# Kernel tuning notes

Hardware: AMD Instinct MI355X
Metric: run time of the kernel (lower is better)

The kernel has to match this reference:

```python
import jax, jax.numpy as jnp
import numpy as np

N_HEADS = 16


def setup_inputs() -> dict:
    key = jax.random.key(0)
    k1, k2, k3 = jax.random.split(key, 3)
    dim = 1024
    # ragged batch: 16 sequences with lengths 64..1024 (step 64), total_nnz = 8704
    lengths = np.arange(64, 1025, 64, dtype=np.int32)  # (16,)
    cu_seqlens = jnp.asarray(np.concatenate([[0], np.cumsum(lengths)]), dtype=jnp.int32)  # (17,)
    total_nnz = int(lengths.sum())  # 8704
    max_seqlen = int(lengths.max())  # 1024
    hidden_states = jax.random.normal(k1, (total_nnz, dim), dtype=jnp.float32)
    # nn.Linear(dim, 3*dim): weight (3*dim, dim), bias (3*dim)
    Wqkv_weight = jax.random.normal(k2, (3 * dim, dim), dtype=jnp.float32) * (dim ** -0.5)
    Wqkv_bias = jax.random.normal(k3, (3 * dim,), dtype=jnp.float32) * 0.02
    return {
        "hidden_states": hidden_states,
        "Wqkv_weight": Wqkv_weight,
        "Wqkv_bias": Wqkv_bias,
        "cu_seqlens": cu_seqlens,
        "max_seqlen": max_seqlen,
    }


def reference(hidden_states, Wqkv_weight, Wqkv_bias, cu_seqlens, max_seqlen):
    # Unpadded (varlen) self-attention, p_dropout = 0 (eval path).
    nnz, dim = hidden_states.shape
    H = N_HEADS
    D = dim // H
    S = int(max_seqlen)  # static pad length
    B = cu_seqlens.shape[0] - 1

    qkv = hidden_states @ Wqkv_weight.T + Wqkv_bias          # (nnz, 3*dim)
    qkv = qkv.reshape(nnz, 3, H, D)

    seqlens = cu_seqlens[1:] - cu_seqlens[:-1]                # (B,)
    pos = jnp.arange(S)
    valid = pos[None, :] < seqlens[:, None]                   # (B, S) token validity
    gather_idx = jnp.where(valid, cu_seqlens[:-1, None] + pos[None, :], 0)

    qkv_pad = qkv[gather_idx]                                 # (B, S, 3, H, D)
    q = qkv_pad[:, :, 0]                                      # (B, S, H, D)
    k = qkv_pad[:, :, 1]
    v = qkv_pad[:, :, 2]

    scale = 1.0 / jnp.sqrt(jnp.asarray(D, dtype=q.dtype))
    scores = jnp.einsum("bshd,bthd->bhst", q, k) * scale      # (B, H, S, S)
    neg_inf = jnp.asarray(-1e9, dtype=scores.dtype)
    scores = jnp.where(valid[:, None, None, :], scores, neg_inf)  # mask invalid keys
    attn = jax.nn.softmax(scores, axis=-1)
    out_pad = jnp.einsum("bhst,bthd->bshd", attn, v)          # (B, S, H, D)

    # scatter back to unpadded layout (nnz, H*D)
    tok = jnp.arange(nnz)
    tok_b = jnp.searchsorted(cu_seqlens, tok, side="right") - 1
    tok_s = tok - cu_seqlens[tok_b]
    out = out_pad[tok_b, tok_s].reshape(nnz, H * D)
    return out
```

## Files before the change

### kernel.cpp

```cpp
#include <hip/hip_runtime.h>
#include <math.h>


#define HD 64

typedef _Float16 half8 __attribute__((ext_vector_type(8)));
typedef _Float16 half4v __attribute__((ext_vector_type(4)));
typedef float f32x4 __attribute__((ext_vector_type(4)));

#define GLP(p) ((__attribute__((address_space(1))) void*)(p))
#define LDSP(p) ((__attribute__((address_space(3))) void*)(p))

__global__ __launch_bounds__(256)
void cvt_kernel(const float* __restrict__ A, const float* __restrict__ W,
                _Float16* __restrict__ Ah, _Float16* __restrict__ Wh,
                int nA4, int nW4)
{
    int total = nA4 + nW4;
    for (int i = blockIdx.x * blockDim.x + threadIdx.x; i < total;
         i += gridDim.x * blockDim.x) {
        const float* src; _Float16* dst; int j;
        if (i < nA4) { src = A; dst = Ah; j = i; }
        else         { src = W; dst = Wh; j = i - nA4; }
        float4 v = *(const float4*)(src + (size_t)j * 4);
        half4v h;
        h.x = (_Float16)v.x; h.y = (_Float16)v.y;
        h.z = (_Float16)v.z; h.w = (_Float16)v.w;
        *(half4v*)(dst + (size_t)j * 4) = h;
    }
}

__global__ __launch_bounds__(256)
void qkv_gemm_kernel(const _Float16* __restrict__ Ah, const _Float16* __restrict__ Wh,
                     const float* __restrict__ bias,
                     _Float16* __restrict__ Qo, _Float16* __restrict__ Ko,
                     _Float16* __restrict__ Vo,
                     int Kd, int dim)
{
    const int bm = blockIdx.x, bn = blockIdx.y;
    const int t = threadIdx.x;
    const int wid = t >> 6, lane = t & 63;
    const int wr = wid >> 1, wc = wid & 1;
    const int fr = lane & 15, fq = lane >> 4;

    __shared__ _Float16 As[128 * 64];
    __shared__ _Float16 Bs[128 * 64];

    const int m0 = bm * 128, n0 = bn * 128;

    f32x4 acc[4][4];
#pragma unroll
    for (int m = 0; m < 4; ++m)
#pragma unroll
        for (int n = 0; n < 4; ++n) acc[m][n] = (f32x4)0.f;

    float biasv[4];
#pragma unroll
    for (int n = 0; n < 4; ++n)
        biasv[n] = bias[n0 + wc * 64 + n * 16 + fr];

    int srow[4], slb[4];
#pragma unroll
    for (int i = 0; i < 4; ++i) {
        int c = t + 256 * i;
        srow[i] = c >> 3;
        slb[i]  = ((c & 7) << 4) ^ ((srow[i] & 7) << 4);
    }

    for (int k0 = 0; k0 < Kd; k0 += 64) {
        __syncthreads();
        {
            const char* Ab = (const char*)Ah + ((size_t)m0 * Kd + k0) * 2;
            const char* Bb = (const char*)Wh + ((size_t)n0 * Kd + k0) * 2;
#pragma unroll
            for (int i = 0; i < 4; ++i) {
                int phys = (t + 256 * i) * 16;
                __builtin_amdgcn_global_load_lds(GLP(Ab + (size_t)srow[i] * Kd * 2 + slb[i]),
                                                 LDSP((char*)As + phys), 16, 0, 0);
                __builtin_amdgcn_global_load_lds(GLP(Bb + (size_t)srow[i] * Kd * 2 + slb[i]),
                                                 LDSP((char*)Bs + phys), 16, 0, 0);
            }
        }
        __syncthreads();

#pragma unroll
        for (int kc = 0; kc < 2; ++kc) {
            half8 a[4], b[4];
#pragma unroll
            for (int m = 0; m < 4; ++m) {
                int row = wr * 64 + m * 16 + fr;
                a[m] = *(const half8*)((const char*)As + row * 128 +
                        ((kc * 64 + fq * 16) ^ ((fr & 7) << 4)));
            }
#pragma unroll
            for (int n = 0; n < 4; ++n) {
                int row = wc * 64 + n * 16 + fr;
                b[n] = *(const half8*)((const char*)Bs + row * 128 +
                        ((kc * 64 + fq * 16) ^ ((fr & 7) << 4)));
            }
#pragma unroll
            for (int m = 0; m < 4; ++m)
#pragma unroll
                for (int n = 0; n < 4; ++n)
                    acc[m][n] = __builtin_amdgcn_mfma_f32_16x16x32_f16(a[m], b[n], acc[m][n], 0, 0, 0);
        }
    }

    const int which = n0 / dim;
    const int offb  = n0 - which * dim;
    _Float16* dst = (which == 0) ? Qo : (which == 1) ? Ko : Vo;
#pragma unroll
    for (int m = 0; m < 4; ++m) {
#pragma unroll
        for (int n = 0; n < 4; ++n) {
            int gc = offb + wc * 64 + n * 16 + fr;
#pragma unroll
            for (int j = 0; j < 4; ++j) {
                int gm = m0 + wr * 64 + m * 16 + fq * 4 + j;
                dst[(size_t)gm * dim + gc] = (_Float16)(acc[m][n][j] + biasv[n]);
            }
        }
    }
}

__global__ __launch_bounds__(256)
void attn_kernel(const _Float16* __restrict__ Q, const _Float16* __restrict__ K,
                 const _Float16* __restrict__ V, const int* __restrict__ cu,
                 float* __restrict__ out, int dim, int H, int B)
{
    const int w  = blockIdx.x;
    const int h  = w & (H - 1);
    const int wq = w / H;

    int b = -1, qt = 0, acc = 0;
    for (int i = B - 1; i >= 0; --i) {
        int Li = cu[i + 1] - cu[i];
        int nq = (Li + 127) >> 7;
        if (wq >= acc && wq < acc + nq) { b = i; qt = wq - acc; }
        acc += nq;
    }
    if (b < 0) return;

    const int s0 = cu[b];
    const int L  = cu[b + 1] - s0;

    const int t    = threadIdx.x;
    const int wid  = t >> 6, lane = t & 63;
    const int fr   = lane & 15, fq = lane >> 4;

    __shared__ _Float16 Ks[64 * 64];
    __shared__ _Float16 Vt[64 * 72];
    __shared__ _Float16 Ps[4][32 * 72];
    __shared__ float    Fs[4][32];

    _Float16* Psw = &Ps[wid][0];
    float*    Fsw = &Fs[wid][0];

    const _Float16 qscale = (_Float16)(0.125f * 1.44269504f);
    half8 aq[2][2];
#pragma unroll
    for (int nt = 0; nt < 2; ++nt)
#pragma unroll
        for (int kc = 0; kc < 2; ++kc) {
            int qrow = qt * 128 + wid * 32 + nt * 16 + fr;
            int qr = (qrow < L) ? qrow : 0;
            half8 v = *(const half8*)(Q + (size_t)(s0 + qr) * dim + h * HD + kc * 32 + fq * 8);
#pragma unroll
            for (int i = 0; i < 8; ++i) v[i] = v[i] * qscale;
            aq[nt][kc] = v;
        }

    f32x4 o[2][4];
    float m2[2], l2[2];
#pragma unroll
    for (int qm = 0; qm < 2; ++qm)
#pragma unroll
        for (int n = 0; n < 4; ++n) o[qm][n] = (f32x4)0.f;
    m2[0] = m2[1] = -3.0e38f;
    l2[0] = l2[1] = 0.f;

    const int nkt = (L + 63) >> 6;
    const int vu = t & 31, vdc = t >> 5;

    for (int kt = 0; kt < nkt; ++kt) {
        __syncthreads();

#pragma unroll
        for (int cc = 0; cc < 2; ++cc) {
            int c    = wid * 2 + cc;
            int phys = c * 1024 + lane * 16;
            int r    = phys >> 7;
            int lb   = (phys & 127) ^ ((r & 7) << 4);
            int krow = kt * 64 + r;
            int kr   = (krow < L) ? krow : 0;
            const char* src = (const char*)K + ((size_t)(s0 + kr) * dim + h * HD) * 2 + lb;
            __builtin_amdgcn_global_load_lds(GLP(src), LDSP((char*)Ks + phys), 16, 0, 0);
        }
        {
            int k0r = kt * 64 + vu * 2;
            int r0 = (k0r     < L) ? k0r     : 0;
            int r1 = (k0r + 1 < L) ? k0r + 1 : 0;
            half8 v0 = *(const half8*)(V + (size_t)(s0 + r0) * dim + h * HD + vdc * 8);
            half8 v1 = *(const half8*)(V + (size_t)(s0 + r1) * dim + h * HD + vdc * 8);
#pragma unroll
            for (int i = 0; i < 8; ++i) {
                union { _Float16 h[2]; unsigned u; } pk;
                pk.h[0] = v0[i]; pk.h[1] = v1[i];
                *(unsigned*)&Vt[(vdc * 8 + i) * 72 + vu * 2] = pk.u;
            }
        }
        __syncthreads();

        f32x4 s2[4][2];
#pragma unroll
        for (int mt = 0; mt < 4; ++mt)
#pragma unroll
            for (int nt = 0; nt < 2; ++nt) s2[mt][nt] = (f32x4)0.f;

#pragma unroll
        for (int mt = 0; mt < 4; ++mt)
#pragma unroll
            for (int kc = 0; kc < 2; ++kc) {
                const half8 bk = *(const half8*)((const char*)Ks +
                    ((mt * 16 + fr) << 7) + (((kc << 6) + (fq << 4)) ^ ((fr & 7) << 4)));
                s2[mt][0] = __builtin_amdgcn_mfma_f32_16x16x32_f16(bk, aq[0][kc], s2[mt][0], 0, 0, 0);
                s2[mt][1] = __builtin_amdgcn_mfma_f32_16x16x32_f16(bk, aq[1][kc], s2[mt][1], 0, 0, 0);
            }

        int ksz = L - kt * 64;
        if (ksz < 64) {
#pragma unroll
            for (int mt = 0; mt < 4; ++mt)
#pragma unroll
                for (int j = 0; j < 4; ++j)
                    if (mt * 16 + fq * 4 + j >= ksz) {
                        s2[mt][0][j] = -1.0e30f;
                        s2[mt][1][j] = -1.0e30f;
                    }
        }

#pragma unroll
        for (int nt = 0; nt < 2; ++nt) {
            f32x4 mx4 = s2[0][nt];
#pragma unroll
            for (int mt = 1; mt < 4; ++mt) {
#pragma unroll
                for (int j = 0; j < 4; ++j) mx4[j] = fmaxf(mx4[j], s2[mt][nt][j]);
            }
            float mx = fmaxf(fmaxf(mx4[0], mx4[1]), fmaxf(mx4[2], mx4[3]));
            mx = fmaxf(mx, __shfl_xor(mx, 16));
            mx = fmaxf(mx, __shfl_xor(mx, 32));
            float mnew = fmaxf(m2[nt], mx);
            float facn = __builtin_exp2f(m2[nt] - mnew);
            m2[nt] = mnew;

            f32x4 sum4 = (f32x4)0.f;
#pragma unroll
            for (int mt = 0; mt < 4; ++mt) {
                half4v ph;
#pragma unroll
                for (int j = 0; j < 4; ++j) {
                    float p = __builtin_exp2f(s2[mt][nt][j] - mnew);
                    sum4[j] += p;
                    ph[j] = (_Float16)p;
                }
                *(half4v*)&Psw[(nt * 16 + fr) * 72 + mt * 16 + fq * 4] = ph;
            }
            float ls = (sum4[0] + sum4[1]) + (sum4[2] + sum4[3]);
            ls += __shfl_xor(ls, 16);
            ls += __shfl_xor(ls, 32);
            l2[nt] = l2[nt] * facn + ls;
            if (fq == 0) Fsw[nt * 16 + fr] = facn;
        }

#pragma unroll
        for (int qm = 0; qm < 2; ++qm) {
            f32x4 fj = *(const f32x4*)&Fsw[qm * 16 + fq * 4];
#pragma unroll
            for (int n2 = 0; n2 < 4; ++n2)
#pragma unroll
                for (int j = 0; j < 4; ++j) o[qm][n2][j] *= fj[j];
        }

#pragma unroll
        for (int kc = 0; kc < 2; ++kc) {
            half8 ap0 = *(const half8*)&Psw[(0 * 16 + fr) * 72 + kc * 32 + fq * 8];
            half8 ap1 = *(const half8*)&Psw[(1 * 16 + fr) * 72 + kc * 32 + fq * 8];
#pragma unroll
            for (int n2 = 0; n2 < 4; ++n2) {
                half8 bv = *(const half8*)&Vt[(n2 * 16 + fr) * 72 + kc * 32 + fq * 8];
                o[0][n2] = __builtin_amdgcn_mfma_f32_16x16x32_f16(ap0, bv, o[0][n2], 0, 0, 0);
                o[1][n2] = __builtin_amdgcn_mfma_f32_16x16x32_f16(ap1, bv, o[1][n2], 0, 0, 0);
            }
        }
    }

    if (fq == 0) { Fsw[fr] = l2[0]; Fsw[16 + fr] = l2[1]; }
#pragma unroll
    for (int qm = 0; qm < 2; ++qm) {
        f32x4 lj = *(const f32x4*)&Fsw[qm * 16 + fq * 4];
#pragma unroll
        for (int j = 0; j < 4; ++j) {
            int qrow = qt * 128 + wid * 32 + qm * 16 + fq * 4 + j;
            if (qrow >= L) continue;
            float inv = 1.0f / lj[j];
#pragma unroll
            for (int n2 = 0; n2 < 4; ++n2)
                out[(size_t)(s0 + qrow) * dim + h * HD + n2 * 16 + fr] = o[qm][n2][j] * inv;
        }
    }
}

extern "C" void kernel_launch(void* const* d_in, const int* in_sizes, int n_in,
                              void* d_out, int out_size, void* d_ws, size_t ws_size,
                              hipStream_t stream)
{
    const float* hs   = (const float*)d_in[0];
    const float* W    = (const float*)d_in[1];
    const float* bias = (const float*)d_in[2];
    const int*   cu   = (const int*)d_in[3];

    const int dim3x = in_sizes[2];
    const int dim   = dim3x / 3;
    const int nnz   = in_sizes[0] / dim;
    const int B     = in_sizes[3] - 1;
    const int H     = dim / HD;
    const size_t nA = (size_t)nnz * dim;
    const size_t nW = (size_t)dim3x * dim;

    _Float16* Ah = (_Float16*)d_ws;
    _Float16* Wh = Ah + nA;
    _Float16* Qh = Wh + nW;
    _Float16* Kh = Qh + nA;
    _Float16* Vh = Kh + nA;

    cvt_kernel<<<1024, 256, 0, stream>>>(hs, W, Ah, Wh, (int)(nA / 4), (int)(nW / 4));

    dim3 g1(nnz / 128, dim3x / 128);
    qkv_gemm_kernel<<<g1, 256, 0, stream>>>(Ah, Wh, bias, Qh, Kh, Vh, dim, dim);

    const int maxWQ = nnz / 128 + B;
    attn_kernel<<<maxWQ * H, 256, 0, stream>>>(Qh, Kh, Vh, cu, (float*)d_out, dim, H, B);
}
```

Before: 244.3 us.

## Read K directly from global, prefetch V in registers, and skip most rescales

Result: slower. 263.2 us (+7.7%).

```diff
diff --git a/kernel.cpp b/kernel.cpp
--- a/kernel.cpp
+++ b/kernel.cpp
@@ -148,7 +148,6 @@
     const int wid  = t >> 6, lane = t & 63;
     const int fr   = lane & 15, fq = lane >> 4;
 
-    __shared__ _Float16 Ks[64 * 64];
     __shared__ _Float16 Vt[64 * 72];
     __shared__ _Float16 Ps[4][32 * 72];
     __shared__ float    Fs[4][32];
@@ -181,33 +180,25 @@
 
     const int nkt = (L + 63) >> 6;
     const int vu = t & 31, vdc = t >> 5;
+    const _Float16* Kbase = K + (size_t)s0 * dim + h * HD;
+    const _Float16* Vbase = V + (size_t)s0 * dim + h * HD + vdc * 8;
+
+    half8 va, vb;
+    {
+        int r0 = vu * 2, r1 = vu * 2 + 1;
+        r0 = (r0 < L) ? r0 : L - 1;  r1 = (r1 < L) ? r1 : L - 1;
+        va = *(const half8*)(Vbase + (size_t)r0 * dim);
+        vb = *(const half8*)(Vbase + (size_t)r1 * dim);
+    }
 
     for (int kt = 0; kt < nkt; ++kt) {
         __syncthreads();
 
 #pragma unroll
-        for (int cc = 0; cc < 2; ++cc) {
-            int c    = wid * 2 + cc;
-            int phys = c * 1024 + lane * 16;
-            int r    = phys >> 7;
-            int lb   = (phys & 127) ^ ((r & 7) << 4);
-            int krow = kt * 64 + r;
-            int kr   = (krow < L) ? krow : 0;
-            const char* src = (const char*)K + ((size_t)(s0 + kr) * dim + h * HD) * 2 + lb;
-            __builtin_amdgcn_global_load_lds(GLP(src), LDSP((char*)Ks + phys), 16, 0, 0);
-        }
-        {
-            int k0r = kt * 64 + vu * 2;
-            int r0 = (k0r     < L) ? k0r     : 0;
-            int r1 = (k0r + 1 < L) ? k0r + 1 : 0;
-            half8 v0 = *(const half8*)(V + (size_t)(s0 + r0) * dim + h * HD + vdc * 8);
-            half8 v1 = *(const half8*)(V + (size_t)(s0 + r1) * dim + h * HD + vdc * 8);
-#pragma unroll
-            for (int i = 0; i < 8; ++i) {
-                union { _Float16 h[2]; unsigned u; } pk;
-                pk.h[0] = v0[i]; pk.h[1] = v1[i];
-                *(unsigned*)&Vt[(vdc * 8 + i) * 72 + vu * 2] = pk.u;
-            }
+        for (int i = 0; i < 8; ++i) {
+            union { _Float16 h[2]; unsigned u; } pk;
+            pk.h[0] = va[i]; pk.h[1] = vb[i];
+            *(unsigned*)&Vt[(vdc * 8 + i) * 72 + vu * 2] = pk.u;
         }
         __syncthreads();
 
@@ -218,14 +209,17 @@
             for (int nt = 0; nt < 2; ++nt) s2[mt][nt] = (f32x4)0.f;
 
 #pragma unroll
-        for (int mt = 0; mt < 4; ++mt)
+        for (int mt = 0; mt < 4; ++mt) {
+            int krow = kt * 64 + mt * 16 + fr;
+            int kr   = (krow < L) ? krow : L - 1;
+            const _Float16* kp = Kbase + (size_t)kr * dim + fq * 8;
 #pragma unroll
             for (int kc = 0; kc < 2; ++kc) {
-                const half8 bk = *(const half8*)((const char*)Ks +
-                    ((mt * 16 + fr) << 7) + (((kc << 6) + (fq << 4)) ^ ((fr & 7) << 4)));
+                const half8 bk = *(const half8*)(kp + kc * 32);
                 s2[mt][0] = __builtin_amdgcn_mfma_f32_16x16x32_f16(bk, aq[0][kc], s2[mt][0], 0, 0, 0);
                 s2[mt][1] = __builtin_amdgcn_mfma_f32_16x16x32_f16(bk, aq[1][kc], s2[mt][1], 0, 0, 0);
             }
+        }
 
         int ksz = L - kt * 64;
         if (ksz < 64) {
@@ -239,28 +233,48 @@
                     }
         }
 
+        float mxv[2];
 #pragma unroll
         for (int nt = 0; nt < 2; ++nt) {
             f32x4 mx4 = s2[0][nt];
 #pragma unroll
-            for (int mt = 1; mt < 4; ++mt) {
+            for (int mt = 1; mt < 4; ++mt)
 #pragma unroll
                 for (int j = 0; j < 4; ++j) mx4[j] = fmaxf(mx4[j], s2[mt][nt][j]);
-            }
             float mx = fmaxf(fmaxf(mx4[0], mx4[1]), fmaxf(mx4[2], mx4[3]));
             mx = fmaxf(mx, __shfl_xor(mx, 16));
             mx = fmaxf(mx, __shfl_xor(mx, 32));
-            float mnew = fmaxf(m2[nt], mx);
-            float facn = __builtin_exp2f(m2[nt] - mnew);
-            m2[nt] = mnew;
-
+            mxv[nt] = mx;
+        }
+        bool need = __any(mxv[0] > m2[0] + 8.f) || __any(mxv[1] > m2[1] + 8.f);
+        if (need) {
+#pragma unroll
+            for (int nt = 0; nt < 2; ++nt) {
+                float mnew = fmaxf(m2[nt], mxv[nt]);
+                float facn = __builtin_exp2f(m2[nt] - mnew);
+                m2[nt] = mnew;
+                l2[nt] *= facn;
+                if (fq == 0) Fsw[nt * 16 + fr] = facn;
+            }
+#pragma unroll
+            for (int qm = 0; qm < 2; ++qm) {
+                f32x4 fj = *(const f32x4*)&Fsw[qm * 16 + fq * 4];
+#pragma unroll
+                for (int n2 = 0; n2 < 4; ++n2)
+#pragma unroll
+                    for (int j = 0; j < 4; ++j) o[qm][n2][j] *= fj[j];
+            }
+        }
+
+#pragma unroll
+        for (int nt = 0; nt < 2; ++nt) {
             f32x4 sum4 = (f32x4)0.f;
 #pragma unroll
             for (int mt = 0; mt < 4; ++mt) {
                 half4v ph;
 #pragma unroll
                 for (int j = 0; j < 4; ++j) {
-                    float p = __builtin_exp2f(s2[mt][nt][j] - mnew);
+                    float p = __builtin_exp2f(s2[mt][nt][j] - m2[nt]);
                     sum4[j] += p;
                     ph[j] = (_Float16)p;
                 }
@@ -269,17 +283,14 @@
             float ls = (sum4[0] + sum4[1]) + (sum4[2] + sum4[3]);
             ls += __shfl_xor(ls, 16);
             ls += __shfl_xor(ls, 32);
-            l2[nt] = l2[nt] * facn + ls;
-            if (fq == 0) Fsw[nt * 16 + fr] = facn;
-        }
-
-#pragma unroll
-        for (int qm = 0; qm < 2; ++qm) {
-            f32x4 fj = *(const f32x4*)&Fsw[qm * 16 + fq * 4];
-#pragma unroll
-            for (int n2 = 0; n2 < 4; ++n2)
-#pragma unroll
-                for (int j = 0; j < 4; ++j) o[qm][n2][j] *= fj[j];
+            l2[nt] += ls;
+        }
+
+        if (kt + 1 < nkt) {
+            int r0 = (kt + 1) * 64 + vu * 2, r1 = r0 + 1;
+            r0 = (r0 < L) ? r0 : L - 1;  r1 = (r1 < L) ? r1 : L - 1;
+            va = *(const half8*)(Vbase + (size_t)r0 * dim);
+            vb = *(const half8*)(Vbase + (size_t)r1 * dim);
         }
 
 #pragma unroll
```
